# Optimization experiments

Measured on AMD Instinct MI355X. Metric: run time of the kernel, lower is better.

## Reference

```python
import jax, jax.numpy as jnp
import numpy as np

THRESHOLD = 0.5
EPS = 1e-6


def setup_inputs() -> dict:
    key = jax.random.key(0)
    k1, k2 = jax.random.split(key)
    points = jax.random.normal(k1, (16, 10, 30, 2), dtype=jnp.float32)
    polys = jax.random.normal(k2, (16, 16, 200, 2), dtype=jnp.float32)
    return {"points": points, "drivable_multipolygon": polys}


def reference(points, drivable_multipolygon):
    # points: (B, C, T, 2); drivable_multipolygon: (B, K, N, 2)
    # Broadcast layout: (B, K, C, T, N-1, ...)
    ps = drivable_multipolygon[:, :, None, None, :-1, :]   # edge starts (B,K,1,1,N-1,2)
    pe = drivable_multipolygon[:, :, None, None, 1:, :]    # edge ends   (B,K,1,1,N-1,2)
    pts = points[:, None, :, :, None, :]                   # (B,1,C,T,1,2)

    # --- point-to-segment distance ---
    v1 = pts - ps
    ev = pe - ps
    dot = jnp.sum(v1 * ev, axis=-1)
    esq = jnp.sum(ev * ev, axis=-1)
    proj = jnp.clip(dot / (esq + EPS), 0.0, 1.0)
    closest = ev * proj[..., None] + ps
    dist_sq = jnp.maximum(jnp.sum((pts - closest) ** 2, axis=-1), EPS)
    min_dist = jnp.min(jnp.sqrt(dist_sq), axis=-1)         # min over edges N-1 -> (B,K,C,T)
    min_dist = jnp.min(min_dist, axis=1)                   # min over polygons K -> (B,C,T)

    # --- ray-casting inside test (parity of crossings) ---
    py = pts[..., 1]
    px = pts[..., 0]
    sy, sx = ps[..., 1], ps[..., 0]
    ey, ex = pe[..., 1], pe[..., 0]
    cond_y = ((sy <= py) & (py < ey)) | ((ey <= py) & (py < sy))
    slope = (ey - sy) / (ex - sx + EPS)
    intersect_x = sx + (py - sy) / (slope + EPS)
    is_left = intersect_x > px
    intersection = cond_y & is_left                        # (B,K,C,T,N-1)
    crossings = jnp.sum(jnp.sum(intersection.astype(jnp.int32), axis=-1), axis=1)  # (B,C,T)
    inside = (crossings % 2) == 1

    min_dist = jnp.where(inside, -min_dist, min_dist)
    min_dist = jax.nn.relu(min_dist + THRESHOLD)
    return jnp.sum(min_dist, axis=-1)                      # (B, C)
```

## Files before the change

kernel.cpp:

```cpp
#include <hip/hip_runtime.h>
#include <math.h>
#include <float.h>

#define EPS 1e-6f
#define THRESHOLD 0.5f

#define NB 16
#define NPOLY 16
#define NVERT 200
#define NSEG_PER_POLY 199
#define NSEG (NPOLY * NSEG_PER_POLY)
#define NPOINTS 4800

__global__ __launch_bounds__(256) void precompute_kernel(
    const float* __restrict__ polys,
    float4* __restrict__ table,
    float* __restrict__ out)
{
    const int idx = blockIdx.x * 256 + threadIdx.x;
    if (idx < 160) out[idx] = 0.0f;
    if (idx >= NB * NSEG) return;

    const int b = idx / NSEG;
    const int s = idx % NSEG;
    const int m = s / NSEG_PER_POLY;
    const int v = s % NSEG_PER_POLY;

    const float2* poly = (const float2*)polys + ((size_t)(b * NPOLY + m) * NVERT);
    const float2 S = poly[v];
    const float2 E = poly[v + 1];

    const float evx = E.x - S.x;
    const float evy = E.y - S.y;
    const float esq = evx * evx + evy * evy;
    const float inv_esq = 1.0f / (esq + EPS);
    const float slope = evy / (evx + EPS);
    const float slope_eps = slope + EPS;

    table[idx * 2]     = make_float4(S.x, S.y, evx, evy);
    table[idx * 2 + 1] = make_float4(inv_esq, slope_eps, E.y, 0.0f);
}

__global__ __launch_bounds__(256) void offroad_kernel(
    const float* __restrict__ points,
    const float4* __restrict__ table,
    float* __restrict__ out)
{
    const int wave = threadIdx.x >> 6;
    const int lane = threadIdx.x & 63;
    const int i = blockIdx.x * 4 + wave;
    const int b   = i / 300;
    const int a   = (i % 300) / 30;

    const float2 pt = *(const float2*)(points + (size_t)i * 2);
    const float px = pt.x, py = pt.y;

    const float4* tb = table + (size_t)b * NSEG * 2;

    float min_dsq = FLT_MAX;
    int crossings = 0;

    #pragma unroll 2
    for (int s = lane; s < NSEG; s += 64) {
        const float4 p0 = tb[s * 2];
        const float4 p1 = tb[s * 2 + 1];
        const float sx = p0.x, sy = p0.y, evx = p0.z, evy = p0.w;
        const float inv_esq = p1.x, slope_eps = p1.y, ey = p1.z;

        const float v1x = px - sx;
        const float v1y = py - sy;
        const float dot = v1x * evx + v1y * evy;
        float t = dot * inv_esq;
        t = fminf(fmaxf(t, 0.0f), 1.0f);
        const float dx = px - (evx * t + sx);
        const float dy = py - (evy * t + sy);
        const float dsq = dx * dx + dy * dy;
        min_dsq = fminf(min_dsq, dsq);

        const bool cond_y = ((sy <= py) & (py < ey)) | ((ey <= py) & (py < sy));
        const float ix = sx + v1y / slope_eps;
        crossings += (cond_y & (ix > px)) ? 1 : 0;
    }

    for (int off = 32; off > 0; off >>= 1) {
        min_dsq   = fminf(min_dsq, __shfl_xor(min_dsq, off));
        crossings += __shfl_xor(crossings, off);
    }

    if (lane == 0) {
        float md = sqrtf(fmaxf(min_dsq, EPS));
        if (crossings & 1) md = -md;
        const float val = fmaxf(md + THRESHOLD, 0.0f);
        atomicAdd(out + (b * 10 + a), val);
    }
}

extern "C" void kernel_launch(void* const* d_in, const int* in_sizes, int n_in,
                              void* d_out, int out_size, void* d_ws, size_t ws_size,
                              hipStream_t stream) {
    const float* points = (const float*)d_in[0];
    const float* polys  = (const float*)d_in[1];
    float* out = (float*)d_out;
    float4* table = (float4*)d_ws;

    const int n_entries = NB * NSEG;
    precompute_kernel<<<(n_entries + 255) / 256, 256, 0, stream>>>(polys, table, out);
    offroad_kernel<<<NPOINTS / 4, 256, 0, stream>>>(points, table, out);
}
```

Measured before the change: 83.79 us.

## Split segment loop into slices per batch with points per thread and final reduction

Restructures the main kernel so each block handles one batch and a slice of 50 segments, with each thread owning one point and looping over the slice. Segment table loads become uniform across the block, so they are broadcast instead of each lane reading a different segment. Per-slice partial minima and crossing counts go to workspace and a third kernel reduces them. This adds a kernel launch and partial-result traffic. The crossing condition is also simplified to a single comparison of two booleans.

```diff
diff --git a/kernel.cpp b/kernel.cpp
--- a/kernel.cpp
+++ b/kernel.cpp
@@ -10,7 +10,10 @@
 #define NVERT 200
 #define NSEG_PER_POLY 199
 #define NSEG (NPOLY * NSEG_PER_POLY)
+#define NPTB 300
 #define NPOINTS 4800
+#define NSLICE 64
+#define SEG_PER_SLICE 50
 
 __global__ __launch_bounds__(256) void precompute_kernel(
     const float* __restrict__ polys,
@@ -34,34 +37,36 @@
     const float evy = E.y - S.y;
     const float esq = evx * evx + evy * evy;
     const float inv_esq = 1.0f / (esq + EPS);
-    const float slope = evy / (evx + EPS);
-    const float slope_eps = slope + EPS;
+    const float slope_eps = evy / (evx + EPS) + EPS;
 
     table[idx * 2]     = make_float4(S.x, S.y, evx, evy);
     table[idx * 2 + 1] = make_float4(inv_esq, slope_eps, E.y, 0.0f);
 }
 
-__global__ __launch_bounds__(256) void offroad_kernel(
+__global__ __launch_bounds__(320) void seg_kernel(
     const float* __restrict__ points,
     const float4* __restrict__ table,
-    float* __restrict__ out)
+    float* __restrict__ part_dsq,
+    int* __restrict__ part_cross)
 {
-    const int wave = threadIdx.x >> 6;
-    const int lane = threadIdx.x & 63;
-    const int i = blockIdx.x * 4 + wave;
-    const int b   = i / 300;
-    const int a   = (i % 300) / 30;
+    const int slice = blockIdx.x;
+    const int b     = blockIdx.y;
+    const int lp    = threadIdx.x;
+    const bool active = lp < NPTB;
 
-    const float2 pt = *(const float2*)(points + (size_t)i * 2);
+    const int pidx = b * NPTB + (active ? lp : 0);
+    const float2 pt = *(const float2*)(points + (size_t)pidx * 2);
     const float px = pt.x, py = pt.y;
 
     const float4* tb = table + (size_t)b * NSEG * 2;
+    const int s0 = slice * SEG_PER_SLICE;
+    const int s1 = (s0 + SEG_PER_SLICE < NSEG) ? s0 + SEG_PER_SLICE : NSEG;
 
     float min_dsq = FLT_MAX;
     int crossings = 0;
 
     #pragma unroll 2
-    for (int s = lane; s < NSEG; s += 64) {
+    for (int s = s0; s < s1; ++s) {
         const float4 p0 = tb[s * 2];
         const float4 p1 = tb[s * 2 + 1];
         const float sx = p0.x, sy = p0.y, evx = p0.z, evy = p0.w;
@@ -77,22 +82,41 @@
         const float dsq = dx * dx + dy * dy;
         min_dsq = fminf(min_dsq, dsq);
 
-        const bool cond_y = ((sy <= py) & (py < ey)) | ((ey <= py) & (py < sy));
+        const bool cond_y = (sy <= py) != (ey <= py);
         const float ix = sx + v1y / slope_eps;
-        crossings += (cond_y & (ix > px)) ? 1 : 0;
+        crossings += (cond_y && (ix > px)) ? 1 : 0;
     }
 
-    for (int off = 32; off > 0; off >>= 1) {
-        min_dsq   = fminf(min_dsq, __shfl_xor(min_dsq, off));
-        crossings += __shfl_xor(crossings, off);
+    if (active) {
+        const int o = slice * NPOINTS + pidx;
+        part_dsq[o]   = min_dsq;
+        part_cross[o] = crossings;
+    }
+}
+
+__global__ __launch_bounds__(256) void final_kernel(
+    const float* __restrict__ part_dsq,
+    const int* __restrict__ part_cross,
+    float* __restrict__ out)
+{
+    const int p = blockIdx.x * 256 + threadIdx.x;
+    if (p >= NPOINTS) return;
+
+    float md = FLT_MAX;
+    int c = 0;
+    #pragma unroll 8
+    for (int k = 0; k < NSLICE; ++k) {
+        md = fminf(md, part_dsq[k * NPOINTS + p]);
+        c += part_cross[k * NPOINTS + p];
     }
 
-    if (lane == 0) {
-        float md = sqrtf(fmaxf(min_dsq, EPS));
-        if (crossings & 1) md = -md;
-        const float val = fmaxf(md + THRESHOLD, 0.0f);
-        atomicAdd(out + (b * 10 + a), val);
-    }
+    float d = sqrtf(fmaxf(md, EPS));
+    if (c & 1) d = -d;
+    const float val = fmaxf(d + THRESHOLD, 0.0f);
+
+    const int b = p / NPTB;
+    const int a = (p % NPTB) / 30;
+    atomicAdd(out + b * 10 + a, val);
 }
 
 extern "C" void kernel_launch(void* const* d_in, const int* in_sizes, int n_in,
@@ -101,9 +125,17 @@
     const float* points = (const float*)d_in[0];
     const float* polys  = (const float*)d_in[1];
     float* out = (float*)d_out;
-    float4* table = (float4*)d_ws;
+
+    char* ws = (char*)d_ws;
+    float4* table     = (float4*)ws;
+    float*  part_dsq  = (float*)(ws + (2u << 20));
+    int*    part_cross= (int*)  (ws + (4u << 20));
 
     const int n_entries = NB * NSEG;
     precompute_kernel<<<(n_entries + 255) / 256, 256, 0, stream>>>(polys, table, out);
-    offroad_kernel<<<NPOINTS / 4, 256, 0, stream>>>(points, table, out);
+
+    dim3 grid(NSLICE, NB);
+    seg_kernel<<<grid, 320, 0, stream>>>(points, table, part_dsq, part_cross);
+
+    final_kernel<<<(NPOINTS + 255) / 256, 256, 0, stream>>>(part_dsq, part_cross, out);
 }
```

Result: slower. 87.14 us (+4.0%).
